# Performance work log

Hardware: AMD Instinct MI355X
Metric: run time of the kernel (lower is better)

The kernel has to match this reference:

```python
import jax, jax.numpy as jnp
import numpy as np

B, S, E, H = 2, 2048, 1024, 16
HD = E // H

def setup_inputs() -> dict:
    key = jax.random.key(0)
    ks = jax.random.split(key, 9)
    s = 1.0 / np.sqrt(E)
    inp = {
        'x': jax.random.normal(ks[0], (B, S, E), dtype=jnp.float32),
        'Wq': jax.random.uniform(ks[1], (E, E), jnp.float32, -s, s),
        'bq': jax.random.uniform(ks[2], (E,), jnp.float32, -s, s),
        'Wk': jax.random.uniform(ks[3], (E, E), jnp.float32, -s, s),
        'bk': jax.random.uniform(ks[4], (E,), jnp.float32, -s, s),
        'Wv': jax.random.uniform(ks[5], (E, E), jnp.float32, -s, s),
        'bv': jax.random.uniform(ks[6], (E,), jnp.float32, -s, s),
        'Wo': jax.random.uniform(ks[7], (E, E), jnp.float32, -s, s),
        'bo': jax.random.uniform(ks[8], (E,), jnp.float32, -s, s),
    }
    return inp

def reference(x, Wq, bq, Wk, bk, Wv, bv, Wo, bo):
    # Linear layers: y = x @ W^T + b (torch nn.Linear convention)
    q = x @ Wq.T + bq  # [B,S,E]
    k = x @ Wk.T + bk
    v = x @ Wv.T + bv
    q = q.reshape(B, S, H, HD).transpose(0, 2, 1, 3)  # [B,H,S,hd]
    k = k.reshape(B, S, H, HD).transpose(0, 2, 1, 3)
    v = v.reshape(B, S, H, HD).transpose(0, 2, 1, 3)
    scores = jnp.einsum('bhqd,bhkd->bhqk', q, k) / jnp.sqrt(jnp.float32(HD))
    attn = jax.nn.softmax(scores, axis=-1)
    out = jnp.einsum('bhqk,bhkd->bhqd', attn, v)  # [B,H,S,hd]
    out = out.transpose(0, 2, 1, 3).reshape(B, S, E)
    return out @ Wo.T + bo
```

## Files before the change

kernel.cpp:

```cpp
#include <hip/hip_runtime.h>

#define B_ 2
#define S_ 2048
#define E_ 1024
#define H_ 16
#define HD_ 64
#define M_ (B_ * S_)
#define BH_ (B_ * H_)
#define NROWS (BH_ * S_)

typedef __attribute__((ext_vector_type(8))) _Float16 half8;
typedef __attribute__((ext_vector_type(4))) float f32x4;
typedef __attribute__((ext_vector_type(4))) unsigned short u16x4;
typedef __attribute__((ext_vector_type(8))) unsigned short u16x8;
typedef unsigned short ushort_t;

static __device__ __forceinline__ ushort_t f2h(float f) {
    union { _Float16 h; ushort_t u; } c; c.h = (_Float16)f; return c.u;
}
static __device__ __forceinline__ float h2f(ushort_t u) {
    union { _Float16 h; ushort_t u; } c; c.u = u; return (float)c.h;
}
static __device__ __forceinline__ void gl2lds16(const ushort_t* g, ushort_t* l) {
    __builtin_amdgcn_global_load_lds(
        (const __attribute__((address_space(1))) unsigned int*)g,
        (__attribute__((address_space(3))) unsigned int*)l,
        16, 0, 0);
}

__global__ __launch_bounds__(256)
void conv_pack(const float* __restrict__ x,  const float* __restrict__ Wq,
               const float* __restrict__ Wk, const float* __restrict__ Wv,
               const float* __restrict__ Wo, const float* __restrict__ bq,
               const float* __restrict__ bk, const float* __restrict__ bv,
               ushort_t* __restrict__ xh,  ushort_t* __restrict__ Wqh,
               ushort_t* __restrict__ Wkh, ushort_t* __restrict__ Wvh,
               ushort_t* __restrict__ Woh, float* __restrict__ bcat)
{
    const int NX = (B_ * S_ * E_) / 4;
    const int NW = (E_ * E_) / 4;
    const int total = NX + 4 * NW + 768;
    for (int u = blockIdx.x * blockDim.x + threadIdx.x; u < total;
         u += gridDim.x * blockDim.x) {
        if (u < NX) {
            float4 v = ((const float4*)x)[u];
            u16x4 o = { f2h(v.x), f2h(v.y), f2h(v.z), f2h(v.w) };
            ((u16x4*)xh)[u] = o;
        } else if (u < NX + 4 * NW) {
            int r = (u - NX) >> 18;
            int i = (u - NX) & (NW - 1);
            const float* src = (r == 0) ? Wq : (r == 1) ? Wk : (r == 2) ? Wv : Wo;
            ushort_t*    dst = (r == 0) ? Wqh : (r == 1) ? Wkh : (r == 2) ? Wvh : Woh;
            float4 v = ((const float4*)src)[i];
            u16x4 o = { f2h(v.x), f2h(v.y), f2h(v.z), f2h(v.w) };
            ((u16x4*)dst)[i] = o;
        } else {
            int i = u - NX - 4 * NW;
            int r = i >> 8, ii = i & 255;
            const float* src = (r == 0) ? bq : (r == 1) ? bk : bv;
            ((float4*)bcat)[r * 256 + ii] = ((const float4*)src)[ii];
        }
    }
}

__global__ __launch_bounds__(256)
void gemm_qkv(const ushort_t* __restrict__ Ah, const ushort_t* __restrict__ W0p,
              const ushort_t* __restrict__ W1p, const ushort_t* __restrict__ W2p,
              const float* __restrict__ bias,
              ushort_t* __restrict__ O0, ushort_t* __restrict__ O1,
              ushort_t* __restrict__ O2)
{
    __shared__ ushort_t As[128 * 64];
    __shared__ ushort_t Ws[128 * 64];

    const int nwg = 24 * 32;
    const int b0  = blockIdx.x;
    const int bid = (b0 & 7) * (nwg >> 3) + (b0 >> 3);
    const int bx = bid % 24, by = bid / 24;
    const int m0 = by * 128, n0 = bx * 128;

    const int t = threadIdx.x;
    const int w = t >> 6, lane = t & 63;
    const int g = lane >> 4, qi = lane & 15, sw = qi & 7;
    const int wr = w >> 1, wc = w & 1;

    const int region = n0 >> 10;
    const ushort_t* WA = (region == 0) ? W0p : (region == 1) ? W1p : W2p;
    const int nw0 = n0 & 1023;

    f32x4 acc[4][4];
    #pragma unroll
    for (int i = 0; i < 4; ++i)
        #pragma unroll
        for (int j = 0; j < 4; ++j) acc[i][j] = (f32x4){0.f, 0.f, 0.f, 0.f};

    for (int kt = 0; kt < 16; ++kt) {
        __syncthreads();
        const int k0 = kt * 64;
        #pragma unroll
        for (int it = 0; it < 4; ++it) {
            int idx = (it * 4 + w) * 64 + lane;
            int row = idx >> 3, c8 = idx & 7;
            gl2lds16(&Ah[(size_t)(m0 + row) * E_ + k0 + ((c8 ^ (row & 7)) << 3)],
                     &As[(it * 4 + w) * 512]);
        }
        #pragma unroll
        for (int it = 0; it < 4; ++it) {
            int idx = (it * 4 + w) * 64 + lane;
            int row = idx >> 3, c8 = idx & 7;
            gl2lds16(&WA[(size_t)(nw0 + row) * E_ + k0 + ((c8 ^ (row & 7)) << 3)],
                     &Ws[(it * 4 + w) * 512]);
        }
        __syncthreads();

        #pragma unroll
        for (int h = 0; h < 2; ++h) {
            half8 af[4], wf[4];
            #pragma unroll
            for (int i = 0; i < 4; ++i)
                af[i] = *(const half8*)&As[(wr * 64 + i * 16 + qi) * 64 +
                                           (((h * 4 + g) ^ sw) << 3)];
            #pragma unroll
            for (int j = 0; j < 4; ++j)
                wf[j] = *(const half8*)&Ws[(wc * 64 + j * 16 + qi) * 64 +
                                           (((h * 4 + g) ^ sw) << 3)];
            __builtin_amdgcn_s_setprio(1);
            #pragma unroll
            for (int i = 0; i < 4; ++i)
                #pragma unroll
                for (int j = 0; j < 4; ++j)
                    acc[i][j] = __builtin_amdgcn_mfma_f32_16x16x32_f16(
                        af[i], wf[j], acc[i][j], 0, 0, 0);
            __builtin_amdgcn_s_setprio(0);
        }
    }

    ushort_t* Out = (region == 0) ? O0 : (region == 1) ? O1 : O2;
    const float osc = (region == 0) ? 0.18033688f : 1.0f;
    #pragma unroll
    for (int j = 0; j < 4; ++j) {
        const int n = n0 + wc * 64 + j * 16 + qi;
        const int nn = n & 1023;
        const int hh = nn >> 6, d = nn & 63;
        const float bj = bias[n];
        #pragma unroll
        for (int i = 0; i < 4; ++i)
            #pragma unroll
            for (int r = 0; r < 4; ++r) {
                const int m = m0 + wr * 64 + i * 16 + g * 4 + r;
                const int b = m >> 11, s = m & (S_ - 1);
                Out[(((size_t)(b * H_ + hh)) * S_ + s) * HD_ + d] =
                    f2h((acc[i][j][r] + bj) * osc);
            }
    }
}

__global__ __launch_bounds__(256)
void gemm_out(const ushort_t* __restrict__ Ah, const ushort_t* __restrict__ Wh,
              const float* __restrict__ bo, float* __restrict__ Of)
{
    __shared__ ushort_t As[2][128 * 64];
    __shared__ ushort_t Ws[2][64 * 64];

    const int nwg = 16 * 32;
    const int b0  = blockIdx.x;
    const int bid = (b0 & 7) * (nwg >> 3) + (b0 >> 3);
    const int bx = bid % 16, by = bid / 16;
    const int m0 = by * 128, n0 = bx * 64;

    const int t = threadIdx.x;
    const int w = t >> 6, lane = t & 63;
    const int g = lane >> 4, qi = lane & 15, sw = qi & 7;
    const int wr = w >> 1, wc = w & 1;

    auto stage = [&](int buf, int kt) {
        const int k0 = kt * 64;
        #pragma unroll
        for (int it = 0; it < 4; ++it) {
            int idx = (it * 4 + w) * 64 + lane;
            int row = idx >> 3, c8 = idx & 7;
            gl2lds16(&Ah[(size_t)(m0 + row) * E_ + k0 + ((c8 ^ (row & 7)) << 3)],
                     &As[buf][(it * 4 + w) * 512]);
        }
        #pragma unroll
        for (int it = 0; it < 2; ++it) {
            int idx = (it * 4 + w) * 64 + lane;
            int row = idx >> 3, c8 = idx & 7;
            gl2lds16(&Wh[(size_t)(n0 + row) * E_ + k0 + ((c8 ^ (row & 7)) << 3)],
                     &Ws[buf][(it * 4 + w) * 512]);
        }
    };

    f32x4 acc[4][2];
    #pragma unroll
    for (int i = 0; i < 4; ++i)
        #pragma unroll
        for (int j = 0; j < 2; ++j) acc[i][j] = (f32x4){0.f, 0.f, 0.f, 0.f};

    stage(0, 0);
    __syncthreads();

    for (int kt = 0; kt < 16; ++kt) {
        const int cur = kt & 1;
        if (kt + 1 < 16) stage(cur ^ 1, kt + 1);
        #pragma unroll
        for (int h = 0; h < 2; ++h) {
            half8 af[4], wf[2];
            #pragma unroll
            for (int i = 0; i < 4; ++i)
                af[i] = *(const half8*)&As[cur][(wr * 64 + i * 16 + qi) * 64 +
                                                (((h * 4 + g) ^ sw) << 3)];
            #pragma unroll
            for (int j = 0; j < 2; ++j)
                wf[j] = *(const half8*)&Ws[cur][(wc * 32 + j * 16 + qi) * 64 +
                                                (((h * 4 + g) ^ sw) << 3)];
            __builtin_amdgcn_s_setprio(1);
            #pragma unroll
            for (int i = 0; i < 4; ++i)
                #pragma unroll
                for (int j = 0; j < 2; ++j)
                    acc[i][j] = __builtin_amdgcn_mfma_f32_16x16x32_f16(
                        af[i], wf[j], acc[i][j], 0, 0, 0);
            __builtin_amdgcn_s_setprio(0);
        }
        __syncthreads();
    }

    #pragma unroll
    for (int j = 0; j < 2; ++j) {
        const int n = n0 + wc * 32 + j * 16 + qi;
        const float bj = bo[n];
        #pragma unroll
        for (int i = 0; i < 4; ++i)
            #pragma unroll
            for (int r = 0; r < 4; ++r) {
                const int m = m0 + wr * 64 + i * 16 + g * 4 + r;
                Of[(size_t)m * E_ + n] = acc[i][j][r] + bj;
            }
    }
}

__global__ __launch_bounds__(256)
void attn_mfma(const ushort_t* __restrict__ Qg, const ushort_t* __restrict__ Kg,
               const ushort_t* __restrict__ Vg,
               ushort_t* __restrict__ On, float2* __restrict__ ml)
{
    __shared__ ushort_t Ks[2][64][64];
    __shared__ ushort_t VtT[2][64][64];
    __shared__ ushort_t Ps[4][32][64];

    const int t    = threadIdx.x;
    const int w    = t >> 6;
    const int lane = t & 63;
    const int g    = lane >> 4;
    const int qi   = lane & 15;
    const int sw   = qi & 7;
    const int bh   = blockIdx.y;
    const int q0   = blockIdx.x * 128;
    const int z    = blockIdx.z;
    const int t0   = z * 16, t1 = t0 + 16;
    const size_t base = (size_t)bh * S_ * HD_;
    const int kvg = t >> 4, dg = t & 15;

    auto stageK = [&](int buf, int tile) {
        const size_t nb = base + (size_t)tile * 64 * HD_;
        #pragma unroll
        for (int it = 0; it < 2; ++it) {
            int u = w * 128 + it * 64 + lane;
            int row = u >> 3, c8 = u & 7;
            gl2lds16(&Kg[nb + (size_t)row * HD_ + ((c8 ^ (row & 7)) << 3)],
                     &Ks[buf][0][0] + (size_t)(w * 128 + it * 64) * 8);
        }
    };

    half8 qf[2][2];
    #pragma unroll
    for (int qc = 0; qc < 2; ++qc)
        #pragma unroll
        for (int h = 0; h < 2; ++h)
            qf[qc][h] = *(const half8*)&Qg[base +
                (size_t)(q0 + w * 32 + qc * 16 + qi) * HD_ + (h * 4 + g) * 8];

    stageK(0, t0);
    {
        const size_t nb = base + (size_t)t0 * 64 * HD_;
        u16x4 vv[4];
        #pragma unroll
        for (int j = 0; j < 4; ++j)
            vv[j] = *(const u16x4*)&Vg[nb + (size_t)(kvg * 4 + j) * HD_ + dg * 4];
        #pragma unroll
        for (int i = 0; i < 4; ++i) {
            int d = dg * 4 + i;
            u16x4 wvec = { vv[0][i], vv[1][i], vv[2][i], vv[3][i] };
            *(u16x4*)&VtT[0][d][8 * ((kvg >> 1) ^ (d & 7)) + 4 * (kvg & 1)] = wvec;
        }
    }
    __syncthreads();

    float m_run[2] = { -3.0e38f, -3.0e38f };
    float l_run[2] = { 0.f, 0.f };
    f32x4 oacc[2][4];
    #pragma unroll
    for (int qc = 0; qc < 2; ++qc)
        #pragma unroll
        for (int rb = 0; rb < 4; ++rb) oacc[qc][rb] = (f32x4){0.f, 0.f, 0.f, 0.f};

    for (int tile = t0; tile < t1; ++tile) {
        const int cur = tile & 1;
        const bool has_next = (tile + 1 < t1);

        u16x4 vpre[4];
        if (has_next) {
            stageK(cur ^ 1, tile + 1);
            const size_t nb = base + (size_t)(tile + 1) * 64 * HD_;
            #pragma unroll
            for (int j = 0; j < 4; ++j)
                vpre[j] = *(const u16x4*)&Vg[nb + (size_t)(kvg * 4 + j) * HD_ + dg * 4];
        }

        f32x4 sacc[2][4];
        #pragma unroll
        for (int rb = 0; rb < 4; ++rb) {
            half8 ka0 = *(const half8*)&Ks[cur][rb * 16 + qi][8 * ((0 + g) ^ sw)];
            half8 ka1 = *(const half8*)&Ks[cur][rb * 16 + qi][8 * ((4 + g) ^ sw)];
            #pragma unroll
            for (int qc = 0; qc < 2; ++qc) {
                f32x4 zz = (f32x4){0.f, 0.f, 0.f, 0.f};
                zz = __builtin_amdgcn_mfma_f32_16x16x32_f16(ka0, qf[qc][0], zz, 0, 0, 0);
                zz = __builtin_amdgcn_mfma_f32_16x16x32_f16(ka1, qf[qc][1], zz, 0, 0, 0);
                sacc[qc][rb] = zz;
            }
        }

        #pragma unroll
        for (int qc = 0; qc < 2; ++qc) {
            float smax = sacc[qc][0][0];
            #pragma unroll
            for (int rb = 0; rb < 4; ++rb)
                #pragma unroll
                for (int r = 0; r < 4; ++r) smax = fmaxf(smax, sacc[qc][rb][r]);
            smax = fmaxf(smax, __shfl_xor(smax, 16));
            smax = fmaxf(smax, __shfl_xor(smax, 32));
            if (__any(smax > m_run[qc] + 8.0f)) {
                const float mnew  = fmaxf(m_run[qc], smax);
                const float alpha = exp2f(m_run[qc] - mnew);
                l_run[qc] *= alpha;
                #pragma unroll
                for (int rb = 0; rb < 4; ++rb)
                    #pragma unroll
                    for (int r = 0; r < 4; ++r) oacc[qc][rb][r] *= alpha;
                m_run[qc] = mnew;
            }
            float psum = 0.f;
            #pragma unroll
            for (int rb = 0; rb < 4; ++rb) {
                u16x4 pv;
                #pragma unroll
                for (int r = 0; r < 4; ++r) {
                    float p = exp2f(sacc[qc][rb][r] - m_run[qc]);
                    psum += p;
                    pv[r] = f2h(p);
                }
                int ch = (2 * rb + (g >> 1)) ^ sw;
                *(u16x4*)&Ps[w][qc * 16 + qi][8 * ch + 4 * (g & 1)] = pv;
            }
            psum += __shfl_xor(psum, 16);
            psum += __shfl_xor(psum, 32);
            l_run[qc] += psum;
        }

        #pragma unroll
        for (int kc = 0; kc < 2; ++kc) {
            half8 pf0 = *(const half8*)&Ps[w][qi][8 * ((4 * kc + g) ^ sw)];
            half8 pf1 = *(const half8*)&Ps[w][16 + qi][8 * ((4 * kc + g) ^ sw)];
            #pragma unroll
            for (int rb = 0; rb < 4; ++rb) {
                half8 va = *(const half8*)&VtT[cur][rb * 16 + qi][8 * ((4 * kc + g) ^ sw)];
                oacc[0][rb] = __builtin_amdgcn_mfma_f32_16x16x32_f16(va, pf0, oacc[0][rb], 0, 0, 0);
                oacc[1][rb] = __builtin_amdgcn_mfma_f32_16x16x32_f16(va, pf1, oacc[1][rb], 0, 0, 0);
            }
        }

        if (has_next) {
            #pragma unroll
            for (int i = 0; i < 4; ++i) {
                int d = dg * 4 + i;
                u16x4 wvec = { vpre[0][i], vpre[1][i], vpre[2][i], vpre[3][i] };
                *(u16x4*)&VtT[cur ^ 1][d][8 * ((kvg >> 1) ^ (d & 7)) + 4 * (kvg & 1)] = wvec;
            }
        }
        __syncthreads();
    }

    #pragma unroll
    for (int qc = 0; qc < 2; ++qc) {
        const int qrow = q0 + w * 32 + qc * 16 + qi;
        const float inv = 1.f / l_run[qc];
        const size_t orow = (size_t)z * NROWS * HD_ +
                            ((size_t)bh * S_ + qrow) * HD_;
        #pragma unroll
        for (int rb = 0; rb < 4; ++rb) {
            u16x4 ov;
            #pragma unroll
            for (int r = 0; r < 4; ++r) ov[r] = f2h(oacc[qc][rb][r] * inv);
            *(u16x4*)&On[orow + rb * 16 + g * 4] = ov;
        }
        if (g == 0) {
            float2 v; v.x = m_run[qc]; v.y = l_run[qc];
            ml[(size_t)z * NROWS + (size_t)bh * S_ + qrow] = v;
        }
    }
}

__global__ __launch_bounds__(256)
void attn_combine(const ushort_t* __restrict__ On, const float2* __restrict__ ml,
                  ushort_t* __restrict__ aoh)
{
    const int gid = blockIdx.x * 256 + threadIdx.x;
    const int row = gid >> 2, dp = gid & 3;
    float2 a = ml[row];
    float2 b2 = ml[NROWS + row];
    const float Mx = fmaxf(a.x, b2.x);
    const float w1 = a.y * exp2f(a.x - Mx);
    const float w2 = b2.y * exp2f(b2.x - Mx);
    const float inv = 1.f / (w1 + w2);
    const float c1 = w1 * inv, c2 = w2 * inv;

    const size_t o1 = (size_t)row * HD_ + dp * 16;
    const size_t o2 = (size_t)NROWS * HD_ + o1;
    const int bh = row >> 11, s = row & (S_ - 1);
    const int b = bh >> 4, h = bh & 15;
    ushort_t* dst = &aoh[((size_t)(b * S_ + s)) * E_ + h * HD_ + dp * 16];
    #pragma unroll
    for (int c = 0; c < 2; ++c) {
        u16x8 v1 = *(const u16x8*)&On[o1 + c * 8];
        u16x8 v2 = *(const u16x8*)&On[o2 + c * 8];
        u16x8 o;
        #pragma unroll
        for (int e = 0; e < 8; ++e)
            o[e] = f2h(c1 * h2f(v1[e]) + c2 * h2f(v2[e]));
        *(u16x8*)&dst[c * 8] = o;
    }
}

extern "C" void kernel_launch(void* const* d_in, const int* in_sizes, int n_in,
                              void* d_out, int out_size, void* d_ws, size_t ws_size,
                              hipStream_t stream) {
    const float* x  = (const float*)d_in[0];
    const float* Wq = (const float*)d_in[1];
    const float* bq = (const float*)d_in[2];
    const float* Wk = (const float*)d_in[3];
    const float* bk = (const float*)d_in[4];
    const float* Wv = (const float*)d_in[5];
    const float* bv = (const float*)d_in[6];
    const float* Wo = (const float*)d_in[7];
    const float* bo = (const float*)d_in[8];
    float* out = (float*)d_out;

    const size_t T4 = (size_t)B_ * S_ * E_;
    const size_t W1 = (size_t)E_ * E_;
    ushort_t* xh  = (ushort_t*)d_ws;
    ushort_t* Wqh = xh  + T4;
    ushort_t* Wkh = Wqh + W1;
    ushort_t* Wvh = Wkh + W1;
    ushort_t* Woh = Wvh + W1;
    ushort_t* qh  = Woh + W1;
    ushort_t* kh  = qh  + T4;
    ushort_t* vh  = kh  + T4;
    ushort_t* On  = vh  + T4;
    float2*   ml  = (float2*)(On + 2 * T4);
    float*    bcat = (float*)(ml + 2 * NROWS);
    ushort_t* aoh = xh;

    dim3 blk(256);
    conv_pack<<<2048, blk, 0, stream>>>(x, Wq, Wk, Wv, Wo, bq, bk, bv,
                                        xh, Wqh, Wkh, Wvh, Woh, bcat);

    gemm_qkv<<<24 * 32, blk, 0, stream>>>(xh, Wqh, Wkh, Wvh, bcat, qh, kh, vh);

    dim3 ga(S_ / 128, BH_, 2);
    attn_mfma<<<ga, blk, 0, stream>>>(qh, kh, vh, On, ml);

    attn_combine<<<(NROWS * 4) / 256, blk, 0, stream>>>(On, ml, aoh);

    gemm_out<<<16 * 32, blk, 0, stream>>>(aoh, Woh, bo, out);
}
```

Before: 238.1 us.

## Transpose GEMM MFMA operands for vector stores; compute softmax row sums via MFMA

The QKV and output GEMMs swap MFMA operand order so each lane holds four consecutive output columns. This lets the epilogues use vectorized bias loads and 8/16-byte stores instead of scattered scalar writes. In the attention kernel, the softmax row sum is now accumulated by an extra MFMA against a ones vector, replacing the per-tile shuffle reductions. P packing uses cvt_pkrtz, which rounds toward zero instead of to nearest. The V-transpose LDS swizzle also gains an extra XOR term to reduce bank conflicts on the transposed reads.

```diff
diff --git a/kernel.cpp b/kernel.cpp
--- a/kernel.cpp
+++ b/kernel.cpp
@@ -10,6 +10,7 @@
 #define NROWS (BH_ * S_)
 
 typedef __attribute__((ext_vector_type(8))) _Float16 half8;
+typedef __attribute__((ext_vector_type(2))) __fp16 fp16x2;
 typedef __attribute__((ext_vector_type(4))) float f32x4;
 typedef __attribute__((ext_vector_type(4))) unsigned short u16x4;
 typedef __attribute__((ext_vector_type(8))) unsigned short u16x8;
@@ -20,6 +21,11 @@
 }
 static __device__ __forceinline__ float h2f(ushort_t u) {
     union { _Float16 h; ushort_t u; } c; c.u = u; return (float)c.h;
+}
+static __device__ __forceinline__ unsigned int pk2h(float a, float b) {
+    union { fp16x2 h; unsigned int u; } c;
+    c.h = __builtin_amdgcn_cvt_pkrtz(a, b);
+    return c.u;
 }
 static __device__ __forceinline__ void gl2lds16(const ushort_t* g, ushort_t* l) {
     __builtin_amdgcn_global_load_lds(
@@ -88,11 +94,11 @@
     const ushort_t* WA = (region == 0) ? W0p : (region == 1) ? W1p : W2p;
     const int nw0 = n0 & 1023;
 
-    f32x4 acc[4][4];
-    #pragma unroll
-    for (int i = 0; i < 4; ++i)
-        #pragma unroll
-        for (int j = 0; j < 4; ++j) acc[i][j] = (f32x4){0.f, 0.f, 0.f, 0.f};
+    f32x4 accT[4][4];
+    #pragma unroll
+    for (int j = 0; j < 4; ++j)
+        #pragma unroll
+        for (int i = 0; i < 4; ++i) accT[j][i] = (f32x4){0.f, 0.f, 0.f, 0.f};
 
     for (int kt = 0; kt < 16; ++kt) {
         __syncthreads();
@@ -126,11 +132,11 @@
                                            (((h * 4 + g) ^ sw) << 3)];
             __builtin_amdgcn_s_setprio(1);
             #pragma unroll
-            for (int i = 0; i < 4; ++i)
+            for (int j = 0; j < 4; ++j)
                 #pragma unroll
-                for (int j = 0; j < 4; ++j)
-                    acc[i][j] = __builtin_amdgcn_mfma_f32_16x16x32_f16(
-                        af[i], wf[j], acc[i][j], 0, 0, 0);
+                for (int i = 0; i < 4; ++i)
+                    accT[j][i] = __builtin_amdgcn_mfma_f32_16x16x32_f16(
+                        wf[j], af[i], accT[j][i], 0, 0, 0);
             __builtin_amdgcn_s_setprio(0);
         }
     }
@@ -139,19 +145,21 @@
     const float osc = (region == 0) ? 0.18033688f : 1.0f;
     #pragma unroll
     for (int j = 0; j < 4; ++j) {
-        const int n = n0 + wc * 64 + j * 16 + qi;
-        const int nn = n & 1023;
-        const int hh = nn >> 6, d = nn & 63;
-        const float bj = bias[n];
-        #pragma unroll
-        for (int i = 0; i < 4; ++i)
-            #pragma unroll
-            for (int r = 0; r < 4; ++r) {
-                const int m = m0 + wr * 64 + i * 16 + g * 4 + r;
-                const int b = m >> 11, s = m & (S_ - 1);
-                Out[(((size_t)(b * H_ + hh)) * S_ + s) * HD_ + d] =
-                    f2h((acc[i][j][r] + bj) * osc);
-            }
+        const int nb = n0 + wc * 64 + j * 16 + g * 4;
+        const int nn = nb & 1023;
+        const int hh = nn >> 6, d0 = nn & 63;
+        const float4 b4 = *(const float4*)&bias[nb];
+        #pragma unroll
+        for (int i = 0; i < 4; ++i) {
+            const int m = m0 + wr * 64 + i * 16 + qi;
+            const int b = m >> 11, s = m & (S_ - 1);
+            u16x4 ov;
+            ov[0] = f2h((accT[j][i][0] + b4.x) * osc);
+            ov[1] = f2h((accT[j][i][1] + b4.y) * osc);
+            ov[2] = f2h((accT[j][i][2] + b4.z) * osc);
+            ov[3] = f2h((accT[j][i][3] + b4.w) * osc);
+            *(u16x4*)&Out[(((size_t)(b * H_ + hh)) * S_ + s) * HD_ + d0] = ov;
+        }
     }
 }
 
@@ -191,11 +199,11 @@
         }
     };
 
-    f32x4 acc[4][2];
-    #pragma unroll
-    for (int i = 0; i < 4; ++i)
-        #pragma unroll
-        for (int j = 0; j < 2; ++j) acc[i][j] = (f32x4){0.f, 0.f, 0.f, 0.f};
+    f32x4 accT[2][4];
+    #pragma unroll
+    for (int j = 0; j < 2; ++j)
+        #pragma unroll
+        for (int i = 0; i < 4; ++i) accT[j][i] = (f32x4){0.f, 0.f, 0.f, 0.f};
 
     stage(0, 0);
     __syncthreads();
@@ -216,11 +224,11 @@
                                                 (((h * 4 + g) ^ sw) << 3)];
             __builtin_amdgcn_s_setprio(1);
             #pragma unroll
-            for (int i = 0; i < 4; ++i)
+            for (int j = 0; j < 2; ++j)
                 #pragma unroll
-                for (int j = 0; j < 2; ++j)
-                    acc[i][j] = __builtin_amdgcn_mfma_f32_16x16x32_f16(
-                        af[i], wf[j], acc[i][j], 0, 0, 0);
+                for (int i = 0; i < 4; ++i)
+                    accT[j][i] = __builtin_amdgcn_mfma_f32_16x16x32_f16(
+                        wf[j], af[i], accT[j][i], 0, 0, 0);
             __builtin_amdgcn_s_setprio(0);
         }
         __syncthreads();
@@ -228,15 +236,18 @@
 
     #pragma unroll
     for (int j = 0; j < 2; ++j) {
-        const int n = n0 + wc * 32 + j * 16 + qi;
-        const float bj = bo[n];
-        #pragma unroll
-        for (int i = 0; i < 4; ++i)
-            #pragma unroll
-            for (int r = 0; r < 4; ++r) {
-                const int m = m0 + wr * 64 + i * 16 + g * 4 + r;
-                Of[(size_t)m * E_ + n] = acc[i][j][r] + bj;
-            }
+        const int nb = n0 + wc * 32 + j * 16 + g * 4;
+        const float4 b4 = *(const float4*)&bo[nb];
+        #pragma unroll
+        for (int i = 0; i < 4; ++i) {
+            const int m = m0 + wr * 64 + i * 16 + qi;
+            float4 ov;
+            ov.x = accT[j][i][0] + b4.x;
+            ov.y = accT[j][i][1] + b4.y;
+            ov.z = accT[j][i][2] + b4.z;
+            ov.w = accT[j][i][3] + b4.w;
+            *(float4*)&Of[(size_t)m * E_ + nb] = ov;
+        }
     }
 }
 
@@ -272,6 +283,15 @@
                      &Ks[buf][0][0] + (size_t)(w * 128 + it * 64) * 8);
         }
     };
+    auto writeV = [&](int buf, const u16x4* vv) {
+        #pragma unroll
+        for (int i = 0; i < 4; ++i) {
+            int d = dg * 4 + i;
+            u16x4 wvec = { vv[0][i], vv[1][i], vv[2][i], vv[3][i] };
+            int p = ((kvg >> 1) ^ (d & 7) ^ (d >> 3)) & 7;
+            *(u16x4*)&VtT[buf][d][8 * p + 4 * (kvg & 1)] = wvec;
+        }
+    };
 
     half8 qf[2][2];
     #pragma unroll
@@ -288,22 +308,22 @@
         #pragma unroll
         for (int j = 0; j < 4; ++j)
             vv[j] = *(const u16x4*)&Vg[nb + (size_t)(kvg * 4 + j) * HD_ + dg * 4];
-        #pragma unroll
-        for (int i = 0; i < 4; ++i) {
-            int d = dg * 4 + i;
-            u16x4 wvec = { vv[0][i], vv[1][i], vv[2][i], vv[3][i] };
-            *(u16x4*)&VtT[0][d][8 * ((kvg >> 1) ^ (d & 7)) + 4 * (kvg & 1)] = wvec;
-        }
+        writeV(0, vv);
     }
     __syncthreads();
 
+    const half8 ones = { (_Float16)1, (_Float16)1, (_Float16)1, (_Float16)1,
+                         (_Float16)1, (_Float16)1, (_Float16)1, (_Float16)1 };
+
     float m_run[2] = { -3.0e38f, -3.0e38f };
-    float l_run[2] = { 0.f, 0.f };
+    f32x4 lacc[2];
     f32x4 oacc[2][4];
     #pragma unroll
-    for (int qc = 0; qc < 2; ++qc)
+    for (int qc = 0; qc < 2; ++qc) {
+        lacc[qc] = (f32x4){0.f, 0.f, 0.f, 0.f};
         #pragma unroll
         for (int rb = 0; rb < 4; ++rb) oacc[qc][rb] = (f32x4){0.f, 0.f, 0.f, 0.f};
+    }
 
     for (int tile = t0; tile < t1; ++tile) {
         const int cur = tile & 1;
@@ -344,58 +364,49 @@
             if (__any(smax > m_run[qc] + 8.0f)) {
                 const float mnew  = fmaxf(m_run[qc], smax);
                 const float alpha = exp2f(m_run[qc] - mnew);
-                l_run[qc] *= alpha;
+                #pragma unroll
+                for (int r = 0; r < 4; ++r) lacc[qc][r] *= alpha;
                 #pragma unroll
                 for (int rb = 0; rb < 4; ++rb)
                     #pragma unroll
                     for (int r = 0; r < 4; ++r) oacc[qc][rb][r] *= alpha;
                 m_run[qc] = mnew;
             }
-            float psum = 0.f;
+            const float mq = m_run[qc];
             #pragma unroll
             for (int rb = 0; rb < 4; ++rb) {
-                u16x4 pv;
-                #pragma unroll
-                for (int r = 0; r < 4; ++r) {
-                    float p = exp2f(sacc[qc][rb][r] - m_run[qc]);
-                    psum += p;
-                    pv[r] = f2h(p);
-                }
+                uint2 pw;
+                pw.x = pk2h(exp2f(sacc[qc][rb][0] - mq), exp2f(sacc[qc][rb][1] - mq));
+                pw.y = pk2h(exp2f(sacc[qc][rb][2] - mq), exp2f(sacc[qc][rb][3] - mq));
                 int ch = (2 * rb + (g >> 1)) ^ sw;
-                *(u16x4*)&Ps[w][qc * 16 + qi][8 * ch + 4 * (g & 1)] = pv;
+                *(uint2*)&Ps[w][qc * 16 + qi][8 * ch + 4 * (g & 1)] = pw;
             }
-            psum += __shfl_xor(psum, 16);
-            psum += __shfl_xor(psum, 32);
-            l_run[qc] += psum;
         }
 
         #pragma unroll
         for (int kc = 0; kc < 2; ++kc) {
             half8 pf0 = *(const half8*)&Ps[w][qi][8 * ((4 * kc + g) ^ sw)];
             half8 pf1 = *(const half8*)&Ps[w][16 + qi][8 * ((4 * kc + g) ^ sw)];
+            lacc[0] = __builtin_amdgcn_mfma_f32_16x16x32_f16(ones, pf0, lacc[0], 0, 0, 0);
+            lacc[1] = __builtin_amdgcn_mfma_f32_16x16x32_f16(ones, pf1, lacc[1], 0, 0, 0);
             #pragma unroll
             for (int rb = 0; rb < 4; ++rb) {
-                half8 va = *(const half8*)&VtT[cur][rb * 16 + qi][8 * ((4 * kc + g) ^ sw)];
+                int p = ((4 * kc + g) ^ sw ^ (2 * rb + (qi >> 3))) & 7;
+                half8 va = *(const half8*)&VtT[cur][rb * 16 + qi][8 * p];
                 oacc[0][rb] = __builtin_amdgcn_mfma_f32_16x16x32_f16(va, pf0, oacc[0][rb], 0, 0, 0);
                 oacc[1][rb] = __builtin_amdgcn_mfma_f32_16x16x32_f16(va, pf1, oacc[1][rb], 0, 0, 0);
             }
         }
 
-        if (has_next) {
-            #pragma unroll
-            for (int i = 0; i < 4; ++i) {
-                int d = dg * 4 + i;
-                u16x4 wvec = { vpre[0][i], vpre[1][i], vpre[2][i], vpre[3][i] };
-                *(u16x4*)&VtT[cur ^ 1][d][8 * ((kvg >> 1) ^ (d & 7)) + 4 * (kvg & 1)] = wvec;
-            }
-        }
+        if (has_next) writeV(cur ^ 1, vpre);
         __syncthreads();
     }
 
     #pragma unroll
     for (int qc = 0; qc < 2; ++qc) {
         const int qrow = q0 + w * 32 + qc * 16 + qi;
-        const float inv = 1.f / l_run[qc];
+        const float lsum = lacc[qc][0];
+        const float inv = 1.f / lsum;
         const size_t orow = (size_t)z * NROWS * HD_ +
                             ((size_t)bh * S_ + qrow) * HD_;
         #pragma unroll
@@ -406,7 +417,7 @@
             *(u16x4*)&On[orow + rb * 16 + g * 4] = ov;
         }
         if (g == 0) {
-            float2 v; v.x = m_run[qc]; v.y = l_run[qc];
+            float2 v; v.x = m_run[qc]; v.y = lsum;
             ml[(size_t)z * NROWS + (size_t)bh * S_ + qrow] = v;
         }
     }
```

Measured after the change: 232.9 us. 1.02x faster.
